# Optimization experiments

Measured on AMD Instinct MI355X. Metric: run time of the kernel, lower is better.

The kernel has to match this reference:

```python
import jax, jax.numpy as jnp
import numpy as np

B, S, D = 4, 1568, 1024
H = 16
HD = D // H  # 64


def setup_inputs() -> dict:
    key = jax.random.key(0)
    ks = jax.random.split(key, 9)
    scale = 0.02
    return {
        "hidden_states": jax.random.normal(ks[0], (B, S, D), dtype=jnp.float32),
        "Wq": jax.random.normal(ks[1], (D, D), dtype=jnp.float32) * scale,
        "bq": jnp.zeros((D,), dtype=jnp.float32),
        "Wk": jax.random.normal(ks[2], (D, D), dtype=jnp.float32) * scale,
        "bk": jnp.zeros((D,), dtype=jnp.float32),
        "Wv": jax.random.normal(ks[3], (D, D), dtype=jnp.float32) * scale,
        "bv": jnp.zeros((D,), dtype=jnp.float32),
        "Wp": jax.random.normal(ks[4], (D, D), dtype=jnp.float32) * scale,
        "bp": jnp.zeros((D,), dtype=jnp.float32),
    }


def reference(hidden_states, Wq, bq, Wk, bk, Wv, bv, Wp, bp):
    x = hidden_states  # [B, S, D]
    # Linear projections (torch Linear: x @ W.T + b)
    q = x @ Wq.T + bq
    k = x @ Wk.T + bk
    v = x @ Wv.T + bv
    # split heads: [B, H, S, HD]
    def heads(t):
        return t.reshape(B, S, H, HD).transpose(0, 2, 1, 3)
    q, k, v = heads(q), heads(k), heads(v)
    scale = 1.0 / jnp.sqrt(jnp.asarray(HD, dtype=q.dtype))
    scores = jnp.einsum('bhqd,bhkd->bhqk', q, k) * scale  # [B,H,S,S]
    probs = jax.nn.softmax(scores, axis=-1)
    ctx = jnp.einsum('bhqk,bhkd->bhqd', probs, v)  # [B,H,S,HD]
    ctx = ctx.transpose(0, 2, 1, 3).reshape(B, S, D)
    out = ctx @ Wp.T + bp
    return out
```

## Files before the change

kernel.cpp:

```cpp
#include <hip/hip_runtime.h>
#include <stdint.h>

#define SEQ 1568
#define SEQV 1600
#define DIM 1024
#define NB 4
#define NH 16
#define HD 64

typedef unsigned short u16;
typedef __bf16 bf16x8 __attribute__((ext_vector_type(8)));
typedef __bf16 bf16x4 __attribute__((ext_vector_type(4)));
typedef float f32x4 __attribute__((ext_vector_type(4)));

#define QSCALE 0.18033688011112042f

#define PSTR 72

__device__ __forceinline__ void load_lds16(const u16* g, u16* s) {
  __builtin_amdgcn_global_load_lds((__attribute__((address_space(1))) void*)g,
                                   (__attribute__((address_space(3))) void*)s,
                                   16, 0, 0);
}

#define WAIT_VM(N) asm volatile("s_waitcnt vmcnt(" #N ")" ::: "memory")
#define LGKM0()    asm volatile("s_waitcnt lgkmcnt(0)" ::: "memory")
#define BAR()      do { __builtin_amdgcn_s_barrier(); \
                        __builtin_amdgcn_sched_barrier(0); } while (0)

__global__ __launch_bounds__(256) void cvt_all(
    const float* __restrict__ x,  const float* __restrict__ wq,
    const float* __restrict__ wk, const float* __restrict__ wv,
    const float* __restrict__ wp,
    u16* __restrict__ xb, u16* __restrict__ wqb, u16* __restrict__ wkb,
    u16* __restrict__ wvb, u16* __restrict__ wpb) {
  int i = blockIdx.x * 256 + threadIdx.x;
  const float* src; u16* dst; int off;
  if (i < 1605632)      { src = x;  dst = xb;  off = i; }
  else if (i < 1867776) { src = wq; dst = wqb; off = i - 1605632; }
  else if (i < 2129920) { src = wk; dst = wkb; off = i - 1867776; }
  else if (i < 2392064) { src = wv; dst = wvb; off = i - 2129920; }
  else                  { src = wp; dst = wpb; off = i - 2392064; }
  float4 v = ((const float4*)src)[off];
  union { unsigned long long u; __bf16 h[4]; } o;
  o.h[0] = (__bf16)v.x; o.h[1] = (__bf16)v.y;
  o.h[2] = (__bf16)v.z; o.h[3] = (__bf16)v.w;
  ((unsigned long long*)dst)[off] = o.u;
}

__global__ __launch_bounds__(256) void gemm_qkv(
    const u16* __restrict__ xb,
    const u16* __restrict__ wq, const u16* __restrict__ wk, const u16* __restrict__ wv,
    const float* __restrict__ bq, const float* __restrict__ bk, const float* __restrict__ bv,
    u16* __restrict__ qo, u16* __restrict__ ko, u16* __restrict__ vto) {
  const int bid = blockIdx.x + (blockIdx.y << 3) + blockIdx.z * 416;
  const int logical = (bid & 7) * 156 + (bid >> 3);
  const int byz = logical >> 3;
  const int by  = byz % 52;
  const int z   = byz / 52;
  const int bi  = by / 13;
  const int st  = by % 13;
  const int bn  = (logical & 7) * 128;

  const u16* W = (z == 0) ? wq : (z == 1) ? wk : wv;
  const float* bias = (z == 0) ? bq : (z == 1) ? bk : bv;

  __shared__ __align__(16) u16 sA[3][128 * 32];
  __shared__ __align__(16) u16 sB[3][128 * 32];

  const int tid = threadIdx.x;
  const int wave = tid >> 6;
  const int lane = tid & 63;
  const int l15 = lane & 15;
  const int quad = lane >> 4;
  const int wm = (wave >> 1) * 64;
  const int wn = (wave & 1) * 64;

  const int sr  = lane >> 2;
  const int scs = (((lane & 3) ^ ((lane >> 3) & 3)) << 3);
  const int r0 = wave * 32;

  int ra1 = st * 128 + r0 + sr;       if (ra1 >= SEQ) ra1 = SEQ - 1;
  int ra2 = st * 128 + r0 + 16 + sr;  if (ra2 >= SEQ) ra2 = SEQ - 1;
  const u16* gA1 = xb + (size_t)(bi * SEQ + ra1) * DIM + scs;
  const u16* gA2 = xb + (size_t)(bi * SEQ + ra2) * DIM + scs;
  const u16* gB1 = W + (size_t)(bn + r0 + sr) * DIM + scs;
  const u16* gB2 = gB1 + 16 * DIM;

  f32x4 acc[4][4] = {};
  const int rsw = (l15 >> 1) & 3;

  auto stage = [&](int kk, u16* sAc, u16* sBc) {
    load_lds16(gA1 + kk, sAc + r0 * 32);
    load_lds16(gA2 + kk, sAc + (r0 + 16) * 32);
    load_lds16(gB1 + kk, sBc + r0 * 32);
    load_lds16(gB2 + kk, sBc + (r0 + 16) * 32);
  };

  auto mstep = [&](const u16* sAc, const u16* sBc) {
    bf16x8 a[4], b[4];
#pragma unroll
    for (int mt = 0; mt < 4; mt++)
      a[mt] = *(const bf16x8*)&sAc[(wm + mt * 16 + l15) * 32 + ((quad ^ rsw) << 3)];
#pragma unroll
    for (int nt = 0; nt < 4; nt++)
      b[nt] = *(const bf16x8*)&sBc[(wn + nt * 16 + l15) * 32 + ((quad ^ rsw) << 3)];
#pragma unroll
    for (int mt = 0; mt < 4; mt++)
#pragma unroll
      for (int nt = 0; nt < 4; nt++)
        acc[mt][nt] = __builtin_amdgcn_mfma_f32_16x16x32_bf16(a[mt], b[nt], acc[mt][nt], 0, 0, 0);
  };

  stage(0,  &sA[0][0], &sB[0][0]);
  stage(32, &sA[1][0], &sB[1][0]);
  stage(64, &sA[2][0], &sB[2][0]);

#pragma unroll 1
  for (int t = 0; t < 30; t += 3) {
    WAIT_VM(8); BAR();
    mstep(&sA[0][0], &sB[0][0]);
    LGKM0(); BAR();
    stage((t + 3) * 32, &sA[0][0], &sB[0][0]);

    WAIT_VM(8); BAR();
    mstep(&sA[1][0], &sB[1][0]);
    LGKM0(); BAR();
    stage((t + 4) * 32, &sA[1][0], &sB[1][0]);

    WAIT_VM(8); BAR();
    mstep(&sA[2][0], &sB[2][0]);
    LGKM0(); BAR();
    if (t + 5 < 32) stage((t + 5) * 32, &sA[2][0], &sB[2][0]);
  }
  WAIT_VM(4); BAR();
  mstep(&sA[0][0], &sB[0][0]);
  WAIT_VM(0); BAR();
  mstep(&sA[1][0], &sB[1][0]);

#pragma unroll
  for (int nt = 0; nt < 4; nt++) {
    const int n = bn + wn + nt * 16 + l15;
    const float bia = bias[n];
    const int h = n >> 6, d = n & 63;
#pragma unroll
    for (int mt = 0; mt < 4; mt++) {
      const int sbase = st * 128 + wm + mt * 16 + quad * 4;
#pragma unroll
      for (int r = 0; r < 4; r++) {
        const int s = sbase + r;
        if (s < SEQ) {
          float val = acc[mt][nt][r] + bia;
          if (z == 0) val *= QSCALE;
          const __bf16 o = (__bf16)val;
          if (z == 0)
            *(__bf16*)&qo[(((size_t)(bi * NH + h)) * SEQ + s) * HD + d] = o;
          else if (z == 1)
            *(__bf16*)&ko[(((size_t)(bi * NH + h)) * SEQ + s) * HD + d] = o;
          else
            *(__bf16*)&vto[(((size_t)(bi * NH + h)) * HD + d) * SEQV + s] = o;
        }
      }
    }
  }
}

__global__ __launch_bounds__(256, 4) void attn(
    const u16* __restrict__ q, const u16* __restrict__ k,
    const u16* __restrict__ vt, u16* __restrict__ ctx) {
  const int bid = blockIdx.x;
  const int logical = (bid & 7) * 104 + (bid >> 3);
  const int bh = logical / 13;
  const int qt = logical % 13;
  const int tid = threadIdx.x;
  const int wave = tid >> 6, lane = tid & 63, l15 = lane & 15, quad = lane >> 4;

  __shared__ __align__(16) u16 sK[64 * 64];
  __shared__ __align__(16) u16 sV[64 * 64];
  __shared__ __align__(16) u16 sP[4][32 * PSTR];

  const u16* qh = q + (size_t)bh * (SEQ * HD);
  const u16* kh = k + (size_t)bh * (SEQ * HD);
  const u16* vh = vt + (size_t)bh * (HD * SEQV);

  bf16x8 aq[2][2];
#pragma unroll
  for (int mt = 0; mt < 2; mt++) {
    int qrow = qt * 128 + wave * 32 + mt * 16 + l15;
    int qr = qrow < SEQ ? qrow : SEQ - 1;
    aq[mt][0] = *(const bf16x8*)&qh[(size_t)qr * HD + quad * 8];
    aq[mt][1] = *(const bf16x8*)&qh[(size_t)qr * HD + 32 + quad * 8];
  }

  const __bf16 kOne = (__bf16)1.0f;
  const bf16x8 vone = {kOne, kOne, kOne, kOne, kOne, kOne, kOne, kOne};

  f32x4 o[2][4] = {};
  f32x4 ol[2] = {};

  const int jrow = lane >> 3;
  const int cg = (lane & 7) ^ jrow;
  u16* sPw = sP[wave];
  const int j7 = l15 & 7;

  for (int j0 = 0; j0 < 1536; j0 += 64) {
    __syncthreads();
    load_lds16(&kh[(size_t)(j0 + wave * 16 + jrow) * HD + cg * 8], &sK[(wave * 16) * 64]);
    load_lds16(&kh[(size_t)(j0 + wave * 16 + 8 + jrow) * HD + cg * 8], &sK[(wave * 16 + 8) * 64]);
    load_lds16(&vh[(size_t)(wave * 16 + jrow) * SEQV + j0 + cg * 8], &sV[(wave * 16) * 64]);
    load_lds16(&vh[(size_t)(wave * 16 + 8 + jrow) * SEQV + j0 + cg * 8], &sV[(wave * 16 + 8) * 64]);
    __syncthreads();

#pragma unroll
    for (int mt = 0; mt < 2; mt++) {
      f32x4 s[4];
      __builtin_amdgcn_s_setprio(1);
#pragma unroll
      for (int jt = 0; jt < 4; jt++) {
        const int j = jt * 16 + l15;
        bf16x8 b0 = *(const bf16x8*)&sK[j * 64 + ((quad ^ j7) * 8)];
        bf16x8 b1 = *(const bf16x8*)&sK[j * 64 + (((4 + quad) ^ j7) * 8)];
        f32x4 acc = {};
        acc = __builtin_amdgcn_mfma_f32_16x16x32_bf16(b0, aq[mt][0], acc, 0, 0, 0);
        acc = __builtin_amdgcn_mfma_f32_16x16x32_bf16(b1, aq[mt][1], acc, 0, 0, 0);
        s[jt] = acc;
      }
      __builtin_amdgcn_s_setprio(0);
#pragma unroll
      for (int jt = 0; jt < 4; jt++) {
        bf16x4 pk;
#pragma unroll
        for (int r = 0; r < 4; r++)
          pk[r] = (__bf16)__builtin_exp2f(s[jt][r]);
        *(bf16x4*)&sPw[(mt * 16 + l15) * PSTR + jt * 16 + quad * 4] = pk;
      }
    }

    LGKM0();

    __builtin_amdgcn_s_setprio(1);
#pragma unroll
    for (int kc = 0; kc < 2; kc++) {
      bf16x8 ap0 = *(const bf16x8*)&sPw[l15 * PSTR + kc * 32 + quad * 8];
      bf16x8 ap1 = *(const bf16x8*)&sPw[(16 + l15) * PSTR + kc * 32 + quad * 8];
#pragma unroll
      for (int dt = 0; dt < 4; dt++) {
        const int d7 = l15 & 7;
        bf16x8 bv = *(const bf16x8*)&sV[(dt * 16 + l15) * 64 + (((kc * 4 + quad) ^ d7) * 8)];
        o[0][dt] = __builtin_amdgcn_mfma_f32_16x16x32_bf16(ap0, bv, o[0][dt], 0, 0, 0);
        o[1][dt] = __builtin_amdgcn_mfma_f32_16x16x32_bf16(ap1, bv, o[1][dt], 0, 0, 0);
      }
      ol[0] = __builtin_amdgcn_mfma_f32_16x16x32_bf16(ap0, vone, ol[0], 0, 0, 0);
      ol[1] = __builtin_amdgcn_mfma_f32_16x16x32_bf16(ap1, vone, ol[1], 0, 0, 0);
    }
    __builtin_amdgcn_s_setprio(0);
  }

  {
    const int j0 = 1536;
    __syncthreads();
    if (wave < 2) {
      load_lds16(&kh[(size_t)(j0 + wave * 16 + jrow) * HD + cg * 8], &sK[(wave * 16) * 64]);
      load_lds16(&kh[(size_t)(j0 + wave * 16 + 8 + jrow) * HD + cg * 8], &sK[(wave * 16 + 8) * 64]);
    }
    load_lds16(&vh[(size_t)(wave * 16 + jrow) * SEQV + j0 + cg * 8], &sV[(wave * 16) * 64]);
    load_lds16(&vh[(size_t)(wave * 16 + 8 + jrow) * SEQV + j0 + cg * 8], &sV[(wave * 16 + 8) * 64]);
    __syncthreads();

#pragma unroll
    for (int mt = 0; mt < 2; mt++) {
      f32x4 s[2];
#pragma unroll
      for (int jt = 0; jt < 2; jt++) {
        const int j = jt * 16 + l15;
        bf16x8 b0 = *(const bf16x8*)&sK[j * 64 + ((quad ^ j7) * 8)];
        bf16x8 b1 = *(const bf16x8*)&sK[j * 64 + (((4 + quad) ^ j7) * 8)];
        f32x4 acc = {};
        acc = __builtin_amdgcn_mfma_f32_16x16x32_bf16(b0, aq[mt][0], acc, 0, 0, 0);
        acc = __builtin_amdgcn_mfma_f32_16x16x32_bf16(b1, aq[mt][1], acc, 0, 0, 0);
        s[jt] = acc;
      }
#pragma unroll
      for (int jt = 0; jt < 2; jt++) {
        bf16x4 pk;
#pragma unroll
        for (int r = 0; r < 4; r++)
          pk[r] = (__bf16)__builtin_exp2f(s[jt][r]);
        *(bf16x4*)&sPw[(mt * 16 + l15) * PSTR + jt * 16 + quad * 4] = pk;
      }
    }

    LGKM0();

    {
      bf16x8 ap0 = *(const bf16x8*)&sPw[l15 * PSTR + quad * 8];
      bf16x8 ap1 = *(const bf16x8*)&sPw[(16 + l15) * PSTR + quad * 8];
#pragma unroll
      for (int dt = 0; dt < 4; dt++) {
        const int d7 = l15 & 7;
        bf16x8 bv = *(const bf16x8*)&sV[(dt * 16 + l15) * 64 + ((quad ^ d7) * 8)];
        o[0][dt] = __builtin_amdgcn_mfma_f32_16x16x32_bf16(ap0, bv, o[0][dt], 0, 0, 0);
        o[1][dt] = __builtin_amdgcn_mfma_f32_16x16x32_bf16(ap1, bv, o[1][dt], 0, 0, 0);
      }
      ol[0] = __builtin_amdgcn_mfma_f32_16x16x32_bf16(ap0, vone, ol[0], 0, 0, 0);
      ol[1] = __builtin_amdgcn_mfma_f32_16x16x32_bf16(ap1, vone, ol[1], 0, 0, 0);
    }
  }

  const int bi = bh >> 4, h = bh & 15;
#pragma unroll
  for (int mt = 0; mt < 2; mt++) {
#pragma unroll
    for (int r = 0; r < 4; r++) {
      const int srow = qt * 128 + wave * 32 + mt * 16 + quad * 4 + r;
      if (srow < SEQ) {
        const float inv = 1.0f / ol[mt][r];
#pragma unroll
        for (int dt = 0; dt < 4; dt++)
          *(__bf16*)&ctx[((size_t)(bi * SEQ + srow)) * DIM + h * HD + dt * 16 + l15] =
              (__bf16)(o[mt][dt][r] * inv);
      }
    }
  }
}

__global__ __launch_bounds__(256) void gemm_out(
    const u16* __restrict__ ctx, const u16* __restrict__ wp,
    const float* __restrict__ bp, float* __restrict__ out) {
  const int bid = blockIdx.x;
  const int logical = (bid & 7) * 49 + (bid >> 3);
  const int bm = (logical >> 3) * 128;
  const int bn = (logical & 7) * 128;

  __shared__ __align__(16) u16 sA[3][128 * 32];
  __shared__ __align__(16) u16 sB[3][128 * 32];

  const int tid = threadIdx.x;
  const int wave = tid >> 6;
  const int lane = tid & 63;
  const int l15 = lane & 15;
  const int quad = lane >> 4;
  const int wm = (wave >> 1) * 64;
  const int wn = (wave & 1) * 64;
  const int sr  = lane >> 2;
  const int scs = (((lane & 3) ^ ((lane >> 3) & 3)) << 3);
  const int r0 = wave * 32;

  const u16* gA1 = ctx + (size_t)(bm + r0 + sr) * DIM + scs;
  const u16* gA2 = gA1 + 16 * DIM;
  const u16* gB1 = wp + (size_t)(bn + r0 + sr) * DIM + scs;
  const u16* gB2 = gB1 + 16 * DIM;

  f32x4 acc[4][4] = {};
  const int rsw = (l15 >> 1) & 3;

  auto stage = [&](int kk, u16* sAc, u16* sBc) {
    load_lds16(gA1 + kk, sAc + r0 * 32);
    load_lds16(gA2 + kk, sAc + (r0 + 16) * 32);
    load_lds16(gB1 + kk, sBc + r0 * 32);
    load_lds16(gB2 + kk, sBc + (r0 + 16) * 32);
  };

  auto mstep = [&](const u16* sAc, const u16* sBc) {
    bf16x8 a[4], b[4];
#pragma unroll
    for (int mt = 0; mt < 4; mt++)
      a[mt] = *(const bf16x8*)&sAc[(wm + mt * 16 + l15) * 32 + ((quad ^ rsw) << 3)];
#pragma unroll
    for (int nt = 0; nt < 4; nt++)
      b[nt] = *(const bf16x8*)&sBc[(wn + nt * 16 + l15) * 32 + ((quad ^ rsw) << 3)];
#pragma unroll
    for (int mt = 0; mt < 4; mt++)
#pragma unroll
      for (int nt = 0; nt < 4; nt++)
        acc[mt][nt] = __builtin_amdgcn_mfma_f32_16x16x32_bf16(a[mt], b[nt], acc[mt][nt], 0, 0, 0);
  };

  stage(0,  &sA[0][0], &sB[0][0]);
  stage(32, &sA[1][0], &sB[1][0]);
  stage(64, &sA[2][0], &sB[2][0]);

#pragma unroll 1
  for (int t = 0; t < 30; t += 3) {
    WAIT_VM(8); BAR();
    mstep(&sA[0][0], &sB[0][0]);
    LGKM0(); BAR();
    stage((t + 3) * 32, &sA[0][0], &sB[0][0]);

    WAIT_VM(8); BAR();
    mstep(&sA[1][0], &sB[1][0]);
    LGKM0(); BAR();
    stage((t + 4) * 32, &sA[1][0], &sB[1][0]);

    WAIT_VM(8); BAR();
    mstep(&sA[2][0], &sB[2][0]);
    LGKM0(); BAR();
    if (t + 5 < 32) stage((t + 5) * 32, &sA[2][0], &sB[2][0]);
  }
  WAIT_VM(4); BAR();
  mstep(&sA[0][0], &sB[0][0]);
  WAIT_VM(0); BAR();
  mstep(&sA[1][0], &sB[1][0]);

#pragma unroll
  for (int nt = 0; nt < 4; nt++) {
    const int n = bn + wn + nt * 16 + l15;
    const float bia = bp[n];
#pragma unroll
    for (int mt = 0; mt < 4; mt++) {
      const int mbase = bm + wm + mt * 16 + quad * 4;
#pragma unroll
      for (int r = 0; r < 4; r++)
        out[(size_t)(mbase + r) * DIM + n] = acc[mt][nt][r] + bia;
    }
  }
}

extern "C" void kernel_launch(void* const* d_in, const int* in_sizes, int n_in,
                              void* d_out, int out_size, void* d_ws, size_t ws_size,
                              hipStream_t stream) {
  const float* x  = (const float*)d_in[0];
  const float* Wq = (const float*)d_in[1];
  const float* bq = (const float*)d_in[2];
  const float* Wk = (const float*)d_in[3];
  const float* bk = (const float*)d_in[4];
  const float* Wv = (const float*)d_in[5];
  const float* bv = (const float*)d_in[6];
  const float* Wp = (const float*)d_in[7];
  const float* bp = (const float*)d_in[8];
  float* out = (float*)d_out;

  char* ws = (char*)d_ws;
  u16* xb   = (u16*)(ws + 0);
  u16* wqb  = (u16*)(ws + 12845056);
  u16* wkb  = (u16*)(ws + 14942208);
  u16* wvb  = (u16*)(ws + 17039360);
  u16* wpb  = (u16*)(ws + 19136512);
  u16* qb   = (u16*)(ws + 21233664);
  u16* kb   = (u16*)(ws + 34078720);
  u16* vtb  = (u16*)(ws + 46923776);
  u16* ctxb = (u16*)(ws + 60030976);

  cvt_all<<<10368, 256, 0, stream>>>(x, Wq, Wk, Wv, Wp, xb, wqb, wkb, wvb, wpb);
  gemm_qkv<<<dim3(8, 52, 3), 256, 0, stream>>>(xb, wqb, wkb, wvb, bq, bk, bv, qb, kb, vtb);
  attn<<<832, 256, 0, stream>>>(qb, kb, vtb, ctxb);
  gemm_out<<<392, 256, 0, stream>>>(ctxb, wpb, bp, out);
}
```

Before: 281.2 us.

## Widen QKV GEMM tile to 128x256 over stacked Wq/Wk/Wv weights

The QKV projection now treats the three weight matrices as one contiguous stacked [3072,1024] matrix, which relies on wqb/wkb/wvb being adjacent in the workspace. Each block computes a 128x256 output tile instead of 128x128, with each wave holding a 64x128 accumulator, and the grid is flattened to 624 blocks with a new swizzle. The aim is to double reuse of the loaded A (activation) tile per MFMA step and cut redundant global reads of x. The cost is twice the accumulator registers, more LDS per block, and adjusted vmcnt waits, which could limit occupancy despite the launch-bounds hint of 2.

After: 297.7 us. +5.9%, slower.

```diff
diff --git a/kernel.cpp b/kernel.cpp
--- a/kernel.cpp
+++ b/kernel.cpp
@@ -48,25 +48,23 @@
   ((unsigned long long*)dst)[off] = o.u;
 }
 
-__global__ __launch_bounds__(256) void gemm_qkv(
-    const u16* __restrict__ xb,
-    const u16* __restrict__ wq, const u16* __restrict__ wk, const u16* __restrict__ wv,
+__global__ __launch_bounds__(256, 2) void gemm_qkv(
+    const u16* __restrict__ xb, const u16* __restrict__ wstk,
     const float* __restrict__ bq, const float* __restrict__ bk, const float* __restrict__ bv,
     u16* __restrict__ qo, u16* __restrict__ ko, u16* __restrict__ vto) {
-  const int bid = blockIdx.x + (blockIdx.y << 3) + blockIdx.z * 416;
-  const int logical = (bid & 7) * 156 + (bid >> 3);
-  const int byz = logical >> 3;
-  const int by  = byz % 52;
-  const int z   = byz / 52;
-  const int bi  = by / 13;
-  const int st  = by % 13;
-  const int bn  = (logical & 7) * 128;
-
-  const u16* W = (z == 0) ? wq : (z == 1) ? wk : wv;
+  const int bid = blockIdx.x;
+  const int logical = (bid & 7) * 78 + (bid >> 3);
+  const int ntile = logical % 12;
+  const int mtile = logical / 12;
+  const int bi = mtile / 13;
+  const int st = mtile % 13;
+  const int bn = ntile * 256;
+
+  const int z = bn >> 10;
   const float* bias = (z == 0) ? bq : (z == 1) ? bk : bv;
 
   __shared__ __align__(16) u16 sA[3][128 * 32];
-  __shared__ __align__(16) u16 sB[3][128 * 32];
+  __shared__ __align__(16) u16 sB[3][256 * 32];
 
   const int tid = threadIdx.x;
   const int wave = tid >> 6;
@@ -74,7 +72,7 @@
   const int l15 = lane & 15;
   const int quad = lane >> 4;
   const int wm = (wave >> 1) * 64;
-  const int wn = (wave & 1) * 64;
+  const int wn = (wave & 1) * 128;
 
   const int sr  = lane >> 2;
   const int scs = (((lane & 3) ^ ((lane >> 3) & 3)) << 3);
@@ -84,31 +82,32 @@
   int ra2 = st * 128 + r0 + 16 + sr;  if (ra2 >= SEQ) ra2 = SEQ - 1;
   const u16* gA1 = xb + (size_t)(bi * SEQ + ra1) * DIM + scs;
   const u16* gA2 = xb + (size_t)(bi * SEQ + ra2) * DIM + scs;
-  const u16* gB1 = W + (size_t)(bn + r0 + sr) * DIM + scs;
-  const u16* gB2 = gB1 + 16 * DIM;
-
-  f32x4 acc[4][4] = {};
+  const u16* gB  = wstk + (size_t)(bn + wave * 64 + sr) * DIM + scs;
+  const int dB = wave * 64 * 32;
+
+  f32x4 acc[4][8] = {};
   const int rsw = (l15 >> 1) & 3;
 
   auto stage = [&](int kk, u16* sAc, u16* sBc) {
     load_lds16(gA1 + kk, sAc + r0 * 32);
     load_lds16(gA2 + kk, sAc + (r0 + 16) * 32);
-    load_lds16(gB1 + kk, sBc + r0 * 32);
-    load_lds16(gB2 + kk, sBc + (r0 + 16) * 32);
+#pragma unroll
+    for (int i = 0; i < 4; i++)
+      load_lds16(gB + (size_t)i * 16 * DIM + kk, sBc + dB + i * 16 * 32);
   };
 
   auto mstep = [&](const u16* sAc, const u16* sBc) {
-    bf16x8 a[4], b[4];
+    bf16x8 a[4], b[8];
 #pragma unroll
     for (int mt = 0; mt < 4; mt++)
       a[mt] = *(const bf16x8*)&sAc[(wm + mt * 16 + l15) * 32 + ((quad ^ rsw) << 3)];
 #pragma unroll
-    for (int nt = 0; nt < 4; nt++)
+    for (int nt = 0; nt < 8; nt++)
       b[nt] = *(const bf16x8*)&sBc[(wn + nt * 16 + l15) * 32 + ((quad ^ rsw) << 3)];
 #pragma unroll
     for (int mt = 0; mt < 4; mt++)
 #pragma unroll
-      for (int nt = 0; nt < 4; nt++)
+      for (int nt = 0; nt < 8; nt++)
         acc[mt][nt] = __builtin_amdgcn_mfma_f32_16x16x32_bf16(a[mt], b[nt], acc[mt][nt], 0, 0, 0);
   };
 
@@ -118,31 +117,31 @@
 
 #pragma unroll 1
   for (int t = 0; t < 30; t += 3) {
-    WAIT_VM(8); BAR();
+    WAIT_VM(12); BAR();
     mstep(&sA[0][0], &sB[0][0]);
     LGKM0(); BAR();
     stage((t + 3) * 32, &sA[0][0], &sB[0][0]);
 
-    WAIT_VM(8); BAR();
+    WAIT_VM(12); BAR();
     mstep(&sA[1][0], &sB[1][0]);
     LGKM0(); BAR();
     stage((t + 4) * 32, &sA[1][0], &sB[1][0]);
 
-    WAIT_VM(8); BAR();
+    WAIT_VM(12); BAR();
     mstep(&sA[2][0], &sB[2][0]);
     LGKM0(); BAR();
     if (t + 5 < 32) stage((t + 5) * 32, &sA[2][0], &sB[2][0]);
   }
-  WAIT_VM(4); BAR();
+  WAIT_VM(6); BAR();
   mstep(&sA[0][0], &sB[0][0]);
   WAIT_VM(0); BAR();
   mstep(&sA[1][0], &sB[1][0]);
 
 #pragma unroll
-  for (int nt = 0; nt < 4; nt++) {
-    const int n = bn + wn + nt * 16 + l15;
-    const float bia = bias[n];
-    const int h = n >> 6, d = n & 63;
+  for (int nt = 0; nt < 8; nt++) {
+    const int n1 = (bn & 1023) + wn + nt * 16 + l15;
+    const float bia = bias[n1];
+    const int h = n1 >> 6, d = n1 & 63;
 #pragma unroll
     for (int mt = 0; mt < 4; mt++) {
       const int sbase = st * 128 + wm + mt * 16 + quad * 4;
@@ -442,7 +441,7 @@
   u16* ctxb = (u16*)(ws + 60030976);
 
   cvt_all<<<10368, 256, 0, stream>>>(x, Wq, Wk, Wv, Wp, xb, wqb, wkb, wvb, wpb);
-  gemm_qkv<<<dim3(8, 52, 3), 256, 0, stream>>>(xb, wqb, wkb, wvb, bq, bk, bv, qb, kb, vtb);
+  gemm_qkv<<<624, 256, 0, stream>>>(xb, wqb, bq, bk, bv, qb, kb, vtb);
   attn<<<832, 256, 0, stream>>>(qb, kb, vtb, ctxb);
   gemm_out<<<392, 256, 0, stream>>>(ctxb, wpb, bp, out);
 }
```

## Split attention KV range in two halves with a separate merge kernel

Applied to the files above, without the earlier changes.

Adds a split-K (flash-decoding style) attention path: each query tile's key range is split into two halves processed by separate blocks, doubling the grid from 832 to 1664 blocks. Partial unnormalized outputs and row sums are written in fp32 to workspace, then a merge kernel sums the halves, normalizes, and writes bf16 context. This targets low occupancy and tail effects from only 832 blocks, at the cost of extra fp32 traffic and an extra launch. The new path is used only when the workspace is large enough.

Result: no change. 283.4 us (+0.8%).

```diff
diff --git a/kernel.cpp b/kernel.cpp
--- a/kernel.cpp
+++ b/kernel.cpp
@@ -324,6 +324,195 @@
   }
 }
 
+__global__ __launch_bounds__(256, 4) void attn_split(
+    const u16* __restrict__ q, const u16* __restrict__ k,
+    const u16* __restrict__ vt, float* __restrict__ po, float* __restrict__ pl) {
+  const int bid = blockIdx.x;
+  const int logical = (bid & 7) * 208 + (bid >> 3);
+  const int half = logical & 1;
+  const int bhqt = logical >> 1;
+  const int bh = bhqt / 13;
+  const int qt = bhqt % 13;
+  const int tid = threadIdx.x;
+  const int wave = tid >> 6, lane = tid & 63, l15 = lane & 15, quad = lane >> 4;
+
+  __shared__ __align__(16) u16 sK[64 * 64];
+  __shared__ __align__(16) u16 sV[64 * 64];
+  __shared__ __align__(16) u16 sP[4][32 * PSTR];
+
+  const u16* qh = q + (size_t)bh * (SEQ * HD);
+  const u16* kh = k + (size_t)bh * (SEQ * HD);
+  const u16* vh = vt + (size_t)bh * (HD * SEQV);
+
+  bf16x8 aq[2][2];
+#pragma unroll
+  for (int mt = 0; mt < 2; mt++) {
+    int qrow = qt * 128 + wave * 32 + mt * 16 + l15;
+    int qr = qrow < SEQ ? qrow : SEQ - 1;
+    aq[mt][0] = *(const bf16x8*)&qh[(size_t)qr * HD + quad * 8];
+    aq[mt][1] = *(const bf16x8*)&qh[(size_t)qr * HD + 32 + quad * 8];
+  }
+
+  const __bf16 kOne = (__bf16)1.0f;
+  const bf16x8 vone = {kOne, kOne, kOne, kOne, kOne, kOne, kOne, kOne};
+
+  f32x4 o[2][4] = {};
+  f32x4 ol[2] = {};
+
+  const int jrow = lane >> 3;
+  const int cg = (lane & 7) ^ jrow;
+  u16* sPw = sP[wave];
+  const int j7 = l15 & 7;
+
+  const int jbeg = half ? 768 : 0;
+  const int jend = half ? 1536 : 768;
+
+#pragma unroll 1
+  for (int j0 = jbeg; j0 < jend; j0 += 64) {
+    __syncthreads();
+    load_lds16(&kh[(size_t)(j0 + wave * 16 + jrow) * HD + cg * 8], &sK[(wave * 16) * 64]);
+    load_lds16(&kh[(size_t)(j0 + wave * 16 + 8 + jrow) * HD + cg * 8], &sK[(wave * 16 + 8) * 64]);
+    load_lds16(&vh[(size_t)(wave * 16 + jrow) * SEQV + j0 + cg * 8], &sV[(wave * 16) * 64]);
+    load_lds16(&vh[(size_t)(wave * 16 + 8 + jrow) * SEQV + j0 + cg * 8], &sV[(wave * 16 + 8) * 64]);
+    __syncthreads();
+
+#pragma unroll
+    for (int mt = 0; mt < 2; mt++) {
+      f32x4 s[4];
+      __builtin_amdgcn_s_setprio(1);
+#pragma unroll
+      for (int jt = 0; jt < 4; jt++) {
+        const int j = jt * 16 + l15;
+        bf16x8 b0 = *(const bf16x8*)&sK[j * 64 + ((quad ^ j7) * 8)];
+        bf16x8 b1 = *(const bf16x8*)&sK[j * 64 + (((4 + quad) ^ j7) * 8)];
+        f32x4 acc = {};
+        acc = __builtin_amdgcn_mfma_f32_16x16x32_bf16(b0, aq[mt][0], acc, 0, 0, 0);
+        acc = __builtin_amdgcn_mfma_f32_16x16x32_bf16(b1, aq[mt][1], acc, 0, 0, 0);
+        s[jt] = acc;
+      }
+      __builtin_amdgcn_s_setprio(0);
+#pragma unroll
+      for (int jt = 0; jt < 4; jt++) {
+        bf16x4 pk;
+#pragma unroll
+        for (int r = 0; r < 4; r++)
+          pk[r] = (__bf16)__builtin_exp2f(s[jt][r]);
+        *(bf16x4*)&sPw[(mt * 16 + l15) * PSTR + jt * 16 + quad * 4] = pk;
+      }
+    }
+
+    LGKM0();
+
+    __builtin_amdgcn_s_setprio(1);
+#pragma unroll
+    for (int kc = 0; kc < 2; kc++) {
+      bf16x8 ap0 = *(const bf16x8*)&sPw[l15 * PSTR + kc * 32 + quad * 8];
+      bf16x8 ap1 = *(const bf16x8*)&sPw[(16 + l15) * PSTR + kc * 32 + quad * 8];
+#pragma unroll
+      for (int dt = 0; dt < 4; dt++) {
+        const int d7 = l15 & 7;
+        bf16x8 bv = *(const bf16x8*)&sV[(dt * 16 + l15) * 64 + (((kc * 4 + quad) ^ d7) * 8)];
+        o[0][dt] = __builtin_amdgcn_mfma_f32_16x16x32_bf16(ap0, bv, o[0][dt], 0, 0, 0);
+        o[1][dt] = __builtin_amdgcn_mfma_f32_16x16x32_bf16(ap1, bv, o[1][dt], 0, 0, 0);
+      }
+      ol[0] = __builtin_amdgcn_mfma_f32_16x16x32_bf16(ap0, vone, ol[0], 0, 0, 0);
+      ol[1] = __builtin_amdgcn_mfma_f32_16x16x32_bf16(ap1, vone, ol[1], 0, 0, 0);
+    }
+    __builtin_amdgcn_s_setprio(0);
+  }
+
+  if (half) {
+    const int j0 = 1536;
+    __syncthreads();
+    if (wave < 2) {
+      load_lds16(&kh[(size_t)(j0 + wave * 16 + jrow) * HD + cg * 8], &sK[(wave * 16) * 64]);
+      load_lds16(&kh[(size_t)(j0 + wave * 16 + 8 + jrow) * HD + cg * 8], &sK[(wave * 16 + 8) * 64]);
+    }
+    load_lds16(&vh[(size_t)(wave * 16 + jrow) * SEQV + j0 + cg * 8], &sV[(wave * 16) * 64]);
+    load_lds16(&vh[(size_t)(wave * 16 + 8 + jrow) * SEQV + j0 + cg * 8], &sV[(wave * 16 + 8) * 64]);
+    __syncthreads();
+
+#pragma unroll
+    for (int mt = 0; mt < 2; mt++) {
+      f32x4 s[2];
+#pragma unroll
+      for (int jt = 0; jt < 2; jt++) {
+        const int j = jt * 16 + l15;
+        bf16x8 b0 = *(const bf16x8*)&sK[j * 64 + ((quad ^ j7) * 8)];
+        bf16x8 b1 = *(const bf16x8*)&sK[j * 64 + (((4 + quad) ^ j7) * 8)];
+        f32x4 acc = {};
+        acc = __builtin_amdgcn_mfma_f32_16x16x32_bf16(b0, aq[mt][0], acc, 0, 0, 0);
+        acc = __builtin_amdgcn_mfma_f32_16x16x32_bf16(b1, aq[mt][1], acc, 0, 0, 0);
+        s[jt] = acc;
+      }
+#pragma unroll
+      for (int jt = 0; jt < 2; jt++) {
+        bf16x4 pk;
+#pragma unroll
+        for (int r = 0; r < 4; r++)
+          pk[r] = (__bf16)__builtin_exp2f(s[jt][r]);
+        *(bf16x4*)&sPw[(mt * 16 + l15) * PSTR + jt * 16 + quad * 4] = pk;
+      }
+    }
+
+    LGKM0();
+
+    {
+      bf16x8 ap0 = *(const bf16x8*)&sPw[l15 * PSTR + quad * 8];
+      bf16x8 ap1 = *(const bf16x8*)&sPw[(16 + l15) * PSTR + quad * 8];
+#pragma unroll
+      for (int dt = 0; dt < 4; dt++) {
+        const int d7 = l15 & 7;
+        bf16x8 bv = *(const bf16x8*)&sV[(dt * 16 + l15) * 64 + ((quad ^ d7) * 8)];
+        o[0][dt] = __builtin_amdgcn_mfma_f32_16x16x32_bf16(ap0, bv, o[0][dt], 0, 0, 0);
+        o[1][dt] = __builtin_amdgcn_mfma_f32_16x16x32_bf16(ap1, bv, o[1][dt], 0, 0, 0);
+      }
+      ol[0] = __builtin_amdgcn_mfma_f32_16x16x32_bf16(ap0, vone, ol[0], 0, 0, 0);
+      ol[1] = __builtin_amdgcn_mfma_f32_16x16x32_bf16(ap1, vone, ol[1], 0, 0, 0);
+    }
+  }
+
+  float* pob = po + (size_t)logical * (128 * 64);
+  float* plb = pl + (size_t)logical * 128;
+#pragma unroll
+  for (int mt = 0; mt < 2; mt++) {
+#pragma unroll
+    for (int r = 0; r < 4; r++) {
+      const int rloc = wave * 32 + mt * 16 + quad * 4 + r;
+      if (l15 == 0) plb[rloc] = ol[mt][r];
+#pragma unroll
+      for (int dt = 0; dt < 4; dt++)
+        pob[(size_t)rloc * 64 + dt * 16 + l15] = o[mt][dt][r];
+    }
+  }
+}
+
+__global__ __launch_bounds__(256) void attn_merge(
+    const float* __restrict__ po, const float* __restrict__ pl,
+    u16* __restrict__ ctx) {
+  const int i = blockIdx.x * 256 + threadIdx.x;
+  const int d4  = i & 15;
+  const int row = (i >> 4) & 127;
+  const int bhqt = i >> 11;
+  const int bh = bhqt / 13, qt = bhqt % 13;
+  const int srow = qt * 128 + row;
+  if (srow >= SEQ) return;
+  const size_t b0 = ((size_t)(bhqt * 2) * 128 + row) * 64 + d4 * 4;
+  const size_t b1 = ((size_t)(bhqt * 2 + 1) * 128 + row) * 64 + d4 * 4;
+  const float4 a = *(const float4*)&po[b0];
+  const float4 b = *(const float4*)&po[b1];
+  const float l = pl[(size_t)(bhqt * 2) * 128 + row] +
+                  pl[(size_t)(bhqt * 2 + 1) * 128 + row];
+  const float inv = 1.0f / l;
+  const int bi = bh >> 4, h = bh & 15;
+  union { unsigned long long u; __bf16 x[4]; } oo;
+  oo.x[0] = (__bf16)((a.x + b.x) * inv);
+  oo.x[1] = (__bf16)((a.y + b.y) * inv);
+  oo.x[2] = (__bf16)((a.z + b.z) * inv);
+  oo.x[3] = (__bf16)((a.w + b.w) * inv);
+  *(unsigned long long*)&ctx[((size_t)(bi * SEQ + srow)) * DIM + h * HD + d4 * 4] = oo.u;
+}
+
 __global__ __launch_bounds__(256) void gemm_out(
     const u16* __restrict__ ctx, const u16* __restrict__ wp,
     const float* __restrict__ bp, float* __restrict__ out) {
@@ -440,9 +629,16 @@
   u16* kb   = (u16*)(ws + 34078720);
   u16* vtb  = (u16*)(ws + 46923776);
   u16* ctxb = (u16*)(ws + 60030976);
+  float* po = (float*)(ws + 72876032);
+  float* pl = (float*)(ws + 127401984);
 
   cvt_all<<<10368, 256, 0, stream>>>(x, Wq, Wk, Wv, Wp, xb, wqb, wkb, wvb, wpb);
   gemm_qkv<<<dim3(8, 52, 3), 256, 0, stream>>>(xb, wqb, wkb, wvb, bq, bk, bv, qb, kb, vtb);
-  attn<<<832, 256, 0, stream>>>(qb, kb, vtb, ctxb);
+  if (ws_size >= 128253952ULL) {
+    attn_split<<<1664, 256, 0, stream>>>(qb, kb, vtb, po, pl);
+    attn_merge<<<6656, 256, 0, stream>>>(po, pl, ctxb);
+  } else {
+    attn<<<832, 256, 0, stream>>>(qb, kb, vtb, ctxb);
+  }
   gemm_out<<<392, 256, 0, stream>>>(ctxb, wpb, bp, out);
 }
```
